# Kernel tuning notes

Hardware: AMD Instinct MI355X
Metric: run time of the kernel (lower is better)

The kernel has to match this reference:

```python
import jax, jax.numpy as jnp
import numpy as np

H = 12      # num_heads
EPS = 1e-5  # LayerNorm eps (torch default)


def _ln(x, g, b):
    m = x.mean(-1, keepdims=True)
    v = x.var(-1, keepdims=True)
    return (x - m) * jax.lax.rsqrt(v + EPS) * g + b


def _rot_half(x):
    x1, x2 = x[..., 0::2], x[..., 1::2]
    return jnp.stack((-x2, x1), axis=-1).reshape(x.shape)


def _rope_tables(n, head_dim):
    # rotary-embedding-torch: RotaryEmbedding(dim=head_dim//2, use_xpos=True),
    # theta=10000, scale_base=512. Only first rot=head_dim//2 dims are rotated.
    rot = head_dim // 2
    inv = 1.0 / (10000.0 ** (jnp.arange(0, rot, 2, dtype=jnp.float32) / rot))
    t = jnp.arange(n, dtype=jnp.float32)
    freqs = jnp.repeat(t[:, None] * inv[None, :], 2, axis=-1)  # (n, rot), interleaved
    base = (jnp.arange(0, rot, 2, dtype=jnp.float32) + 0.4 * rot) / (1.4 * rot)
    power = (t - n // 2) / 512.0
    sc = base[None, :] ** power[:, None]
    sc = jnp.concatenate([sc, sc], axis=-1)  # (n, rot), concatenated (library behavior)
    return jnp.cos(freqs), jnp.sin(freqs), sc


def _attn_path(xn, Wqkv, bqkv, Wproj, bproj, qg, qb, kg, kb, R, rg, rb):
    B, N, D = xn.shape
    d = D // H
    qkv = xn @ Wqkv + bqkv
    q, k, v = jnp.split(qkv, 3, axis=-1)
    hd = lambda t: t.reshape(B, N, H, d).transpose(0, 2, 1, 3)  # (B,H,N,d)
    q, k, v = hd(q), hd(k), hd(v)
    q = _ln(q, qg, qb)  # per-head QK LayerNorm
    k = _ln(k, kg, kb)
    cos, sin, sc = _rope_tables(N, d)
    rot = d // 2

    def rope(t, s):  # rotate only first rot dims
        tl, tr = t[..., :rot], t[..., rot:]
        tl = tl * cos * s + _rot_half(tl) * sin * s
        return jnp.concatenate([tl, tr], axis=-1)

    q = rope(q, sc)
    v = rope(v, 1.0 / sc)  # source applies rope to (q, v), not k

    scores = jnp.einsum('bhid,bhjd->bhij', q, k) / jnp.sqrt(jnp.asarray(d, xn.dtype))
    p = jax.nn.softmax(scores, axis=-1)
    # SDPA(q,k,ones_NN)[...,i,j] == sum_k p[...,i,k] for every j (constant over j).
    # All downstream ops (head-mix einsum, LayerNorm over heads, @ v) therefore
    # reduce exactly to the per-(b,i) computation below, avoiding an N^3 matmul.
    s = p.sum(-1)                              # (B,H,N)
    mix = jnp.einsum('bhi,hg->big', s, R)      # (B,N,H)
    w = _ln(mix, rg, rb)                       # reattn LayerNorm over head axis
    vsum = v.sum(axis=2)                       # (B,H,d); (w @ v) with w const over j
    y = jnp.einsum('big,bgd->bigd', w, vsum).reshape(B, N, D)
    return y @ Wproj + bproj


def _cgmlp(xn, W1, b1, gg, gb, cw, cb, W2, b2):
    h = jax.nn.gelu(xn @ W1 + b1, approximate=False)
    c2 = h.shape[-1] // 2
    xr, xg = h[..., :c2], h[..., c2:]
    xg = _ln(xg, gg, gb).transpose(0, 2, 1)  # (B,C,T)
    K = cw.shape[-1]
    xg = jax.lax.conv_general_dilated(xg, cw, (1,), [((K - 1) // 2, (K - 1) // 2)],
                                      dimension_numbers=('NCH', 'OIH', 'NCH'),
                                      feature_group_count=c2)  # depthwise conv1d
    xg = (xg + cb[None, :, None]).transpose(0, 2, 1)
    return (xr * xg) @ W2 + b2


def reference(x, Wqkv, bqkv, Wproj, bproj, qn_g, qn_b, kn_g, kn_b, reattn_w, rn_g, rn_b,
              ln1_g, ln1_b, ln2_g, ln2_b, ls1, ls2, W1, b1, gn_g, gn_b, conv_w, conv_b,
              W2, b2, Wout, bout):
    # eval mode: dropout / drop_path are identity
    xa = _ln(x, ln1_g, ln1_b)
    attn = sum(_attn_path(xa, Wqkv[p], bqkv[p], Wproj[p], bproj[p], qn_g[p], qn_b[p],
                          kn_g[p], kn_b[p], reattn_w[p], rn_g[p], rn_b[p])
               for p in range(2))
    x_attn = x + ls1 * attn
    xm = _ln(x, ln2_g, ln2_b)
    x_mlp = x + ls2 * _cgmlp(xm, W1, b1, gn_g, gn_b, conv_w, conv_b, W2, b2)
    xf = jnp.concatenate([x_attn, x_mlp], axis=-1)
    return xf @ Wout + bout + x


def setup_inputs():
    B, N, D, P = 4, 1024, 768, 2
    d = D // H
    C = 4 * D
    c2 = C // 2
    K = 21
    ks = iter(jax.random.split(jax.random.key(0), 16))
    nrm = lambda s, sd=0.02: jax.random.normal(next(ks), s, jnp.float32) * sd
    return {
        'x': jax.random.normal(next(ks), (B, N, D), jnp.float32),
        'Wqkv': nrm((P, D, 3 * D)), 'bqkv': jnp.zeros((P, 3 * D)),
        'Wproj': nrm((P, D, D)), 'bproj': jnp.zeros((P, D)),
        'qn_g': jnp.ones((P, d)), 'qn_b': jnp.zeros((P, d)),
        'kn_g': jnp.ones((P, d)), 'kn_b': jnp.zeros((P, d)),
        'reattn_w': jax.random.normal(next(ks), (P, H, H), jnp.float32),
        'rn_g': jnp.ones((P, H)), 'rn_b': jnp.zeros((P, H)),
        'ln1_g': jnp.ones((D,)), 'ln1_b': jnp.zeros((D,)),
        'ln2_g': jnp.ones((D,)), 'ln2_b': jnp.zeros((D,)),
        'ls1': jnp.full((D,), 0.01, jnp.float32), 'ls2': jnp.full((D,), 0.01, jnp.float32),
        'W1': nrm((D, C)), 'b1': jnp.zeros((C,)),
        'gn_g': jnp.ones((c2,)), 'gn_b': jnp.zeros((c2,)),
        'conv_w': nrm((c2, 1, K), 0.1), 'conv_b': jnp.zeros((c2,)),
        'W2': nrm((c2, D)), 'b2': jnp.zeros((D,)),
        'Wout': nrm((2 * D, D)), 'bout': jnp.zeros((D,)),
    }
```

## Files before the change

### kernel.cpp

```cpp
#include <hip/hip_runtime.h>
#include <hip/hip_bf16.h>

typedef short s16x8 __attribute__((ext_vector_type(8)));
typedef float f32x4 __attribute__((ext_vector_type(4)));

#define C2 1536

__device__ __forceinline__ float b2f(ushort u){ return __uint_as_float(((unsigned)u)<<16); }
__device__ __forceinline__ ushort f2b(float f){ unsigned u = __float_as_uint(f); return (ushort)((u + 0x7fffu + ((u>>16)&1u)) >> 16); }

template<int EPI>
__global__ __launch_bounds__(256) void gemm_bf16(
    const ushort* __restrict__ A, const ushort* __restrict__ BT,
    int M, int N, int K,
    const float* __restrict__ bias, const float* __restrict__ scale,
    const float* __restrict__ xres,
    ushort* __restrict__ o16, ushort* __restrict__ o16b, float* __restrict__ o32)
{
    __shared__ ushort Al[2][128*32];
    __shared__ ushort Bl[2][128*32];
    const int t = threadIdx.x;
    const int m0 = blockIdx.y*128, n0 = blockIdx.x*128;
    const int lane = t & 63, wv = t >> 6;
    const int wm = (wv>>1)*64, wn = (wv&1)*64;
    const int r0 = lane & 15, q = lane >> 4;

    const int c0i = t, c1i = t + 256;
    const int lrow0 = ((c0i>>6)<<4) | (c0i&15), lkc0 = ((c0i>>4)&3) << 3;
    const int lrow1 = ((c1i>>6)<<4) | (c1i&15), lkc1 = ((c1i>>4)&3) << 3;
    const ushort* gA0 = A  + (size_t)(m0+lrow0)*K + lkc0;
    const ushort* gB0 = BT + (size_t)(n0+lrow0)*K + lkc0;
    const ushort* gA1 = A  + (size_t)(m0+lrow1)*K + lkc1;
    const ushort* gB1 = BT + (size_t)(n0+lrow1)*K + lkc1;

    f32x4 acc[4][4];
    #pragma unroll
    for (int i=0;i<4;++i)
        #pragma unroll
        for (int j=0;j<4;++j) acc[i][j] = (f32x4){0.f,0.f,0.f,0.f};

    const int nkt = K >> 5;
    uint4 pa0_0, pb0_0, pa1_0, pb1_0;
    uint4 pa0_1, pb0_1, pa1_1, pb1_1;
    pa0_0 = *(const uint4*)gA0;        pb0_0 = *(const uint4*)gB0;
    pa1_0 = *(const uint4*)gA1;        pb1_0 = *(const uint4*)gB1;
    pa0_1 = *(const uint4*)(gA0 + 32); pb0_1 = *(const uint4*)(gB0 + 32);
    pa1_1 = *(const uint4*)(gA1 + 32); pb1_1 = *(const uint4*)(gB1 + 32);
    *(uint4*)&Al[0][c0i*8] = pa0_0;
    *(uint4*)&Bl[0][c0i*8] = pb0_0;
    *(uint4*)&Al[0][c1i*8] = pa1_0;
    *(uint4*)&Bl[0][c1i*8] = pb1_0;

    for (int kt = 0; kt < nkt; kt += 2) {
        __syncthreads();
        {
            s16x8 af[4], bfr[4];
            #pragma unroll
            for (int mt=0; mt<4; ++mt) af[mt]  = *(const s16x8*)&Al[0][(((wm>>4)+mt)*64 + lane)*8];
            #pragma unroll
            for (int nt=0; nt<4; ++nt) bfr[nt] = *(const s16x8*)&Bl[0][(((wn>>4)+nt)*64 + lane)*8];
            *(uint4*)&Al[1][c0i*8] = pa0_1;
            *(uint4*)&Bl[1][c0i*8] = pb0_1;
            *(uint4*)&Al[1][c1i*8] = pa1_1;
            *(uint4*)&Bl[1][c1i*8] = pb1_1;
            if (kt+2 < nkt) {
                pa0_0 = *(const uint4*)(gA0 + (kt+2)*32);
                pb0_0 = *(const uint4*)(gB0 + (kt+2)*32);
                pa1_0 = *(const uint4*)(gA1 + (kt+2)*32);
                pb1_0 = *(const uint4*)(gB1 + (kt+2)*32);
            }
            #pragma unroll
            for (int mt=0; mt<4; ++mt)
                #pragma unroll
                for (int nt=0; nt<4; ++nt)
                    acc[mt][nt] = __builtin_amdgcn_mfma_f32_16x16x32_bf16(af[mt], bfr[nt], acc[mt][nt], 0,0,0);
        }
        __syncthreads();
        {
            s16x8 af[4], bfr[4];
            #pragma unroll
            for (int mt=0; mt<4; ++mt) af[mt]  = *(const s16x8*)&Al[1][(((wm>>4)+mt)*64 + lane)*8];
            #pragma unroll
            for (int nt=0; nt<4; ++nt) bfr[nt] = *(const s16x8*)&Bl[1][(((wn>>4)+nt)*64 + lane)*8];
            if (kt+2 < nkt) {
                *(uint4*)&Al[0][c0i*8] = pa0_0;
                *(uint4*)&Bl[0][c0i*8] = pb0_0;
                *(uint4*)&Al[0][c1i*8] = pa1_0;
                *(uint4*)&Bl[0][c1i*8] = pb1_0;
            }
            if (kt+3 < nkt) {
                pa0_1 = *(const uint4*)(gA0 + (kt+3)*32);
                pb0_1 = *(const uint4*)(gB0 + (kt+3)*32);
                pa1_1 = *(const uint4*)(gA1 + (kt+3)*32);
                pb1_1 = *(const uint4*)(gB1 + (kt+3)*32);
            }
            #pragma unroll
            for (int mt=0; mt<4; ++mt)
                #pragma unroll
                for (int nt=0; nt<4; ++nt)
                    acc[mt][nt] = __builtin_amdgcn_mfma_f32_16x16x32_bf16(af[mt], bfr[nt], acc[mt][nt], 0,0,0);
        }
    }

    #pragma unroll
    for (int mt=0; mt<4; ++mt) {
        #pragma unroll
        for (int nt=0; nt<4; ++nt) {
            int col = n0 + wn + nt*16 + r0;
            #pragma unroll
            for (int r=0; r<4; ++r) {
                int row = m0 + wm + mt*16 + q*4 + r;
                float v = acc[mt][nt][r];
                if (EPI == 0) {
                    o16[(size_t)row*N + col] = f2b(v + bias[col]);
                } else if (EPI == 1) {
                    v += bias[col];
                    float g = 0.5f*v*(1.0f + erff(v*0.70710678118f));
                    if (col < C2) o16 [(size_t)row*C2 + col]        = f2b(g);
                    else          o16b[(size_t)row*C2 + (col - C2)] = f2b(g);
                } else if (EPI == 2) {
                    v += bias[col];
                    o16[(size_t)row*1536 + 768 + col] = f2b(xres[(size_t)row*768 + col] + scale[col]*v);
                } else {
                    o32[(size_t)row*768 + col] = v + bias[col] + xres[(size_t)row*768 + col];
                }
            }
        }
    }
}

__global__ __launch_bounds__(256) void pack_bt(const float* __restrict__ src, ushort* __restrict__ dst,
                                               int K, int ld, int coff)
{
    __shared__ float tl[32*33];
    int kt = blockIdx.x*32, nt = blockIdx.y*32;
    int nl = threadIdx.x & 31, kg = threadIdx.x >> 5;
    #pragma unroll
    for (int kk=0; kk<4; ++kk) {
        int k = kg*4 + kk;
        tl[k*33 + nl] = src[(size_t)(kt + k)*ld + coff + nt + nl];
    }
    __syncthreads();
    int kcol = threadIdx.x & 31, ng = threadIdx.x >> 5;
    #pragma unroll
    for (int nn=0; nn<4; ++nn) {
        int nrow = ng*4 + nn;
        dst[(size_t)(nt + nrow)*K + kt + kcol] = f2b(tl[kcol*33 + nrow]);
    }
}

__global__ __launch_bounds__(256) void pack_bv(const float* __restrict__ bqkv, float* __restrict__ bvp)
{
    int idx = blockIdx.x*256 + threadIdx.x;
    if (idx < 1536) bvp[idx] = bqkv[(idx/768)*2304 + 1536 + (idx%768)];
}

__global__ __launch_bounds__(256) void ln_x_kernel(const float* __restrict__ x,
    const float* __restrict__ g1, const float* __restrict__ b1,
    const float* __restrict__ g2, const float* __restrict__ b2,
    ushort* __restrict__ xa, ushort* __restrict__ xm)
{
    __shared__ float sb[8];
    int row = blockIdx.x; int t = threadIdx.x;
    float v[3]; float s = 0.f, ss = 0.f;
    #pragma unroll
    for (int e=0; e<3; ++e) { v[e] = x[(size_t)row*768 + t + e*256]; s += v[e]; ss += v[e]*v[e]; }
    for (int o=32; o>0; o>>=1){ s += __shfl_down(s,o,64); ss += __shfl_down(ss,o,64); }
    int lane = t&63, w = t>>6;
    if (lane==0){ sb[w]=s; sb[4+w]=ss; }
    __syncthreads();
    s = sb[0]+sb[1]+sb[2]+sb[3]; ss = sb[4]+sb[5]+sb[6]+sb[7];
    float mean = s*(1.f/768.f);
    float var  = ss*(1.f/768.f) - mean*mean;
    float rstd = rsqrtf(var + 1e-5f);
    #pragma unroll
    for (int e=0; e<3; ++e){
        int c = t + e*256;
        float n = (v[e]-mean)*rstd;
        xa[(size_t)row*768 + c] = f2b(n*g1[c] + b1[c]);
        xm[(size_t)row*768 + c] = f2b(n*g2[c] + b2[c]);
    }
}

__global__ __launch_bounds__(256) void prep_kernel(
    float* __restrict__ w1t, float* __restrict__ w2t, float* __restrict__ wvec,
    float* __restrict__ attn_c, float* __restrict__ vsum,
    const float* __restrict__ R, const float* __restrict__ rng,
    const float* __restrict__ rnb, const float* __restrict__ bproj)
{
    int idx = blockIdx.x*256 + threadIdx.x;
    {
        int i = idx >> 6, j = idx & 63;
        float w1, w2;
        if (j < 32) {
            int m = j >> 1;
            float inv = powf(10000.f, -(float)m*(1.f/16.f));
            float fr = (float)i * inv;
            float c = cosf(fr), sn = sinf(fr);
            float power = ((float)i - 512.f) * (1.f/512.f);
            float basev = (2.f*(float)(j & 15) + 12.8f) * (1.f/44.8f);
            float sfac = powf(basev, -power);
            w1 = c * sfac;
            w2 = ((j & 1) ? sn : -sn) * sfac;
        } else { w1 = 1.f; w2 = 0.f; }
        w1t[idx] = w1; w2t[idx] = w2;
    }
    if (blockIdx.x >= 1 && blockIdx.x <= 12) {
        int k = (blockIdx.x-1)*256 + threadIdx.x;
        int o = k % 768;
        attn_c[k] = bproj[o] + bproj[768 + o];
    }
    if (blockIdx.x >= 13 && blockIdx.x <= 36) {
        int k = (blockIdx.x-13)*256 + threadIdx.x;
        vsum[k] = 0.f;
    }
    if (blockIdx.x == 0) {
        __shared__ float mixs[24];
        __shared__ float ws[24];
        int t = threadIdx.x;
        if (t < 24) {
            int p = t / 12, g = t % 12;
            float m = 0.f;
            for (int h=0; h<12; ++h) m += R[p*144 + h*12 + g];
            mixs[t] = m;
        }
        __syncthreads();
        if (t < 2) {
            float mean=0.f, var=0.f;
            for (int g=0; g<12; ++g) mean += mixs[t*12+g];
            mean *= (1.f/12.f);
            for (int g=0; g<12; ++g){ float d = mixs[t*12+g]-mean; var += d*d; }
            var *= (1.f/12.f);
            float rstd = rsqrtf(var + 1e-5f);
            for (int g=0; g<12; ++g)
                ws[t*12+g] = (mixs[t*12+g]-mean)*rstd*rng[t*12+g] + rnb[t*12+g];
        }
        __syncthreads();
        if (t < 24) wvec[t] = ws[t];
    }
}

__global__ __launch_bounds__(256) void rope_reduce(const ushort* __restrict__ V,
    const float* __restrict__ w1t, const float* __restrict__ w2t, float* __restrict__ vsum)
{
    int col = blockIdx.x*256 + threadIdx.x;
    int b = blockIdx.y;
    int i0 = blockIdx.z * 256;
    int j = col & 63;
    float acc = 0.f;
    const ushort* vp = V + (size_t)(b*1024 + i0)*1536;
    #pragma unroll 4
    for (int i=0; i<256; ++i) {
        float v1 = b2f(vp[(size_t)i*1536 + col]);
        float v2 = b2f(vp[(size_t)i*1536 + (col^1)]);
        int ii = i0 + i;
        acc += w1t[ii*64 + j]*v1 + w2t[ii*64 + j]*v2;
    }
    atomicAdd(&vsum[b*1536 + col], acc);
}

__global__ __launch_bounds__(256) void attn_gemm(const float* __restrict__ vsum,
    const float* __restrict__ wvec, const float* __restrict__ Wproj, float* __restrict__ attn_c)
{
    int o  = blockIdx.x*256 + threadIdx.x;
    int c0 = blockIdx.y * 96;
    int b  = blockIdx.z;
    int p  = c0 / 768;
    float acc = 0.f;
    #pragma unroll 4
    for (int cc=0; cc<96; ++cc) {
        int c = c0 + cc;
        int cl = c - p*768;
        float y = wvec[p*12 + (cl>>6)] * vsum[b*1536 + c];
        acc += y * Wproj[(size_t)p*589824 + (size_t)cl*768 + o];
    }
    atomicAdd(&attn_c[b*768 + o], acc);
}

__global__ __launch_bounds__(256) void xf_left(const float* __restrict__ x, const float* __restrict__ ls1,
    const float* __restrict__ attn_c, ushort* __restrict__ xf)
{
    int col = blockIdx.x*256 + threadIdx.x;
    int row = blockIdx.y;
    xf[(size_t)row*1536 + col] = f2b(x[(size_t)row*768 + col] + ls1[col]*attn_c[(row>>10)*768 + col]);
}

__global__ __launch_bounds__(256) void ln_gate(const ushort* __restrict__ xg,
    const float* __restrict__ g, const float* __restrict__ bta, ushort* __restrict__ out)
{
    __shared__ float sb[8];
    int row = blockIdx.x, t = threadIdx.x;
    float v[6]; float s=0.f, ss=0.f;
    #pragma unroll
    for (int e=0;e<6;++e){ v[e] = b2f(xg[(size_t)row*1536 + t + e*256]); s+=v[e]; ss+=v[e]*v[e]; }
    for (int o=32; o>0; o>>=1){ s += __shfl_down(s,o,64); ss += __shfl_down(ss,o,64); }
    int lane = t&63, w = t>>6;
    if (lane==0){ sb[w]=s; sb[4+w]=ss; }
    __syncthreads();
    s = sb[0]+sb[1]+sb[2]+sb[3]; ss = sb[4]+sb[5]+sb[6]+sb[7];
    float mean = s*(1.f/1536.f);
    float var  = ss*(1.f/1536.f) - mean*mean;
    float rstd = rsqrtf(var + 1e-5f);
    #pragma unroll
    for (int e=0;e<6;++e){
        int c = t + e*256;
        out[(size_t)row*1536 + c] = f2b((v[e]-mean)*rstd*g[c] + bta[c]);
    }
}

#define CROWS 128
#define CIN   (CROWS + 20)
#define CSTR  72
__global__ __launch_bounds__(256) void conv_mul(const ushort* __restrict__ xgln,
    const float* __restrict__ cw, const float* __restrict__ cb,
    const ushort* __restrict__ xr, ushort* __restrict__ u)
{
    __shared__ ushort tile[CIN * CSTR];
    const int c0 = blockIdx.x * 64;
    const int i0 = blockIdx.y * CROWS;
    const int b  = blockIdx.z;
    const int t  = threadIdx.x;
    const size_t base = (size_t)b*1024*1536;

    #pragma unroll
    for (int it = 0; it < 5; ++it) {
        int idx = it*256 + t;
        if (idx < CIN*8) {
            int r  = idx >> 3;
            int cq = (idx & 7) * 8;
            int si = i0 + r - 10;
            uint4 val = make_uint4(0u,0u,0u,0u);
            if (si >= 0 && si < 1024)
                val = *(const uint4*)(xgln + base + (size_t)si*1536 + c0 + cq);
            *(uint4*)&tile[r*CSTR + cq] = val;
        }
    }
    __syncthreads();

    const int ch = t & 63;
    const int o0 = (t >> 6) * 32;
    const int c  = c0 + ch;

    float w[21];
    #pragma unroll
    for (int k=0; k<21; ++k) w[k] = cw[c*21 + k];
    const float bias = cb[c];

    float win[21];
    #pragma unroll
    for (int j=0; j<20; ++j) win[j] = b2f(tile[(o0+j)*CSTR + ch]);

    #pragma unroll
    for (int j=0; j<32; ++j) {
        win[(j+20)%21] = b2f(tile[(o0+j+20)*CSTR + ch]);
        float acc = bias;
        #pragma unroll
        for (int k=0; k<21; ++k) acc += win[(j+k)%21] * w[k];
        size_t off = base + (size_t)(i0+o0+j)*1536 + c;
        u[off] = f2b(b2f(xr[off]) * acc);
    }
}

extern "C" void kernel_launch(void* const* d_in, const int* in_sizes, int n_in,
                              void* d_out, int out_size, void* d_ws, size_t ws_size,
                              hipStream_t stream)
{
    const float* x     = (const float*)d_in[0];
    const float* Wqkv  = (const float*)d_in[1];
    const float* bqkv  = (const float*)d_in[2];
    const float* Wproj = (const float*)d_in[3];
    const float* bproj = (const float*)d_in[4];
    const float* Rw    = (const float*)d_in[9];
    const float* rng   = (const float*)d_in[10];
    const float* rnb   = (const float*)d_in[11];
    const float* ln1g  = (const float*)d_in[12];
    const float* ln1b  = (const float*)d_in[13];
    const float* ln2g  = (const float*)d_in[14];
    const float* ln2b  = (const float*)d_in[15];
    const float* ls1   = (const float*)d_in[16];
    const float* ls2   = (const float*)d_in[17];
    const float* W1    = (const float*)d_in[18];
    const float* b1    = (const float*)d_in[19];
    const float* gng   = (const float*)d_in[20];
    const float* gnb   = (const float*)d_in[21];
    const float* cw    = (const float*)d_in[22];
    const float* cb    = (const float*)d_in[23];
    const float* W2    = (const float*)d_in[24];
    const float* b2    = (const float*)d_in[25];
    const float* Wout  = (const float*)d_in[26];
    const float* bout  = (const float*)d_in[27];
    float* out = (float*)d_out;

    char* ws = (char*)d_ws;
    size_t off = 0;
    auto alloc = [&](size_t bytes)->char* {
        char* p = ws + off;
        off += (bytes + 255) & ~(size_t)255;
        return p;
    };
    ushort* WvT   = (ushort*)alloc(1536*768*2);
    ushort* W1T   = (ushort*)alloc(3072*768*2);
    ushort* W2T   = (ushort*)alloc(768*1536*2);
    ushort* WoutT = (ushort*)alloc(768*1536*2);
    float*  bvp   = (float*)alloc(1536*4);
    float*  w1t   = (float*)alloc(65536*4);
    float*  w2t   = (float*)alloc(65536*4);
    float*  wvec  = (float*)alloc(24*4);
    float*  attnc = (float*)alloc(3072*4);
    float*  vsum  = (float*)alloc(6144*4);
    ushort* xa16  = (ushort*)alloc(4096*768*2);
    ushort* xm16  = (ushort*)alloc(4096*768*2);
    ushort* V16   = (ushort*)alloc(4096*1536*2);
    ushort* xg16  = (ushort*)alloc(4096*1536*2);
    ushort* xf16  = (ushort*)alloc(4096*1536*2);
    ushort* xgln  = xa16;
    ushort* xr16  = V16;
    ushort* u16   = xg16;
    (void)ws_size; (void)n_in; (void)in_sizes; (void)out_size;

    for (int p = 0; p < 2; ++p)
        pack_bt<<<dim3(24, 24), 256, 0, stream>>>(Wqkv + (size_t)p*768*2304, WvT + (size_t)p*768*768,
                                                  768, 2304, 1536);
    pack_bt<<<dim3(24, 96), 256, 0, stream>>>(W1,   W1T,   768,  3072, 0);
    pack_bt<<<dim3(48, 24), 256, 0, stream>>>(W2,   W2T,   1536, 768,  0);
    pack_bt<<<dim3(48, 24), 256, 0, stream>>>(Wout, WoutT, 1536, 768,  0);
    pack_bv<<<dim3(6), 256, 0, stream>>>(bqkv, bvp);
    prep_kernel<<<dim3(256), 256, 0, stream>>>(w1t, w2t, wvec, attnc, vsum, Rw, rng, rnb, bproj);

    ln_x_kernel<<<dim3(4096), 256, 0, stream>>>(x, ln1g, ln1b, ln2g, ln2b, xa16, xm16);

    gemm_bf16<0><<<dim3(12, 32), 256, 0, stream>>>(xa16, WvT, 4096, 1536, 768,
                                                   bvp, nullptr, nullptr, V16, nullptr, nullptr);
    rope_reduce<<<dim3(6, 4, 4), 256, 0, stream>>>(V16, w1t, w2t, vsum);
    attn_gemm<<<dim3(3, 16, 4), 256, 0, stream>>>(vsum, wvec, Wproj, attnc);
    xf_left<<<dim3(3, 4096), 256, 0, stream>>>(x, ls1, attnc, xf16);

    gemm_bf16<1><<<dim3(24, 32), 256, 0, stream>>>(xm16, W1T, 4096, 3072, 768,
                                                   b1, nullptr, nullptr, xr16, xg16, nullptr);
    ln_gate<<<dim3(4096), 256, 0, stream>>>(xg16, gng, gnb, xgln);
    conv_mul<<<dim3(24, 8, 4), 256, 0, stream>>>(xgln, cw, cb, xr16, u16);
    gemm_bf16<2><<<dim3(6, 32), 256, 0, stream>>>(u16, W2T, 4096, 768, 1536,
                                                  b2, ls2, x, xf16, nullptr, nullptr);
    gemm_bf16<3><<<dim3(6, 32), 256, 0, stream>>>(xf16, WoutT, 4096, 768, 1536,
                                                  bout, nullptr, x, nullptr, nullptr, out);
}
```

Baseline: 363.6 us.

## Add 256x256 tile GEMM with direct global-to-LDS loads for V and W1 projections

Adds a new 512-thread GEMM kernel that computes 256x256 output tiles with K-step 64, loading A and B straight into 128 KB of dynamic LDS through global_load_lds. It uses XOR-swizzled LDS addressing, a hand-written ping-pong pipeline with explicit waitcnt, barriers and setprio, and 8x4 MFMA accumulators per wave. The V projection and the W1+GELU GEMM switch to it, and the old kernel keeps only the residual epilogues. The aim is more operand reuse per loaded byte and overlap of loads with MFMA work. In exchange the grids get much smaller (96 and 192 blocks on a 256-CU part), so fewer CUs are busy, and register use is high.

After: 367.4 us. No clear change (+1.0%).

```diff
diff --git a/kernel.cpp b/kernel.cpp
--- a/kernel.cpp
+++ b/kernel.cpp
@@ -8,6 +8,155 @@
 
 __device__ __forceinline__ float b2f(ushort u){ return __uint_as_float(((unsigned)u)<<16); }
 __device__ __forceinline__ ushort f2b(float f){ unsigned u = __float_as_uint(f); return (ushort)((u + 0x7fffu + ((u>>16)&1u)) >> 16); }
+
+#define GL16(g, l) __builtin_amdgcn_global_load_lds( \
+    (const __attribute__((address_space(1))) void*)(g), \
+    (__attribute__((address_space(3))) void*)(l), 16, 0, 0)
+
+#define VMW(n) asm volatile("s_waitcnt vmcnt(" #n ")" ::: "memory")
+#define LGW()  asm volatile("s_waitcnt lgkmcnt(0)" ::: "memory")
+#define SB()   __builtin_amdgcn_sched_barrier(0)
+#define BAR()  __builtin_amdgcn_s_barrier()
+#define SP1    __builtin_amdgcn_s_setprio(1)
+#define SP0    __builtin_amdgcn_s_setprio(0)
+#define MF(va, vb, c) __builtin_amdgcn_mfma_f32_16x16x32_bf16(va, vb, c, 0,0,0)
+
+#define RDA(P, mh) { const int ab = (P) + aro + (mh)*4096; \
+    a0=L8(ab+sx0);      a1=L8(ab+sx1); \
+    a2=L8(ab+1024+sx0); a3=L8(ab+1024+sx1); \
+    a4=L8(ab+2048+sx0); a5=L8(ab+2048+sx1); \
+    a6=L8(ab+3072+sx0); a7=L8(ab+3072+sx1); }
+#define RDB0(P, nh) { const int bb = (P) + bro + (nh)*2048; \
+    b00=L8(bb+sx0); b01=L8(bb+sx1); b02=L8(bb+1024+sx0); b03=L8(bb+1024+sx1); }
+#define RDB1(P, nh) { const int bb = (P) + bro + (nh)*2048; \
+    b10=L8(bb+sx0); b11=L8(bb+sx1); b12=L8(bb+1024+sx0); b13=L8(bb+1024+sx1); }
+#define L8(off) (*(const s16x8*)&lds[off])
+#define STG(p0, p1, T, dstb) { \
+    GL16((p0) + (size_t)(T)*64, &lds[(dstb) + ldsw]); \
+    GL16((p1) + (size_t)(T)*64, &lds[(dstb) + 4096 + ldsw]); }
+#define QD(mh, nh, B0,B1,B2,B3) { \
+  acc[(mh)*4+0][(nh)*2+0]=MF(a0,B0,acc[(mh)*4+0][(nh)*2+0]); \
+  acc[(mh)*4+0][(nh)*2+0]=MF(a1,B1,acc[(mh)*4+0][(nh)*2+0]); \
+  acc[(mh)*4+0][(nh)*2+1]=MF(a0,B2,acc[(mh)*4+0][(nh)*2+1]); \
+  acc[(mh)*4+0][(nh)*2+1]=MF(a1,B3,acc[(mh)*4+0][(nh)*2+1]); \
+  acc[(mh)*4+1][(nh)*2+0]=MF(a2,B0,acc[(mh)*4+1][(nh)*2+0]); \
+  acc[(mh)*4+1][(nh)*2+0]=MF(a3,B1,acc[(mh)*4+1][(nh)*2+0]); \
+  acc[(mh)*4+1][(nh)*2+1]=MF(a2,B2,acc[(mh)*4+1][(nh)*2+1]); \
+  acc[(mh)*4+1][(nh)*2+1]=MF(a3,B3,acc[(mh)*4+1][(nh)*2+1]); \
+  acc[(mh)*4+2][(nh)*2+0]=MF(a4,B0,acc[(mh)*4+2][(nh)*2+0]); \
+  acc[(mh)*4+2][(nh)*2+0]=MF(a5,B1,acc[(mh)*4+2][(nh)*2+0]); \
+  acc[(mh)*4+2][(nh)*2+1]=MF(a4,B2,acc[(mh)*4+2][(nh)*2+1]); \
+  acc[(mh)*4+2][(nh)*2+1]=MF(a5,B3,acc[(mh)*4+2][(nh)*2+1]); \
+  acc[(mh)*4+3][(nh)*2+0]=MF(a6,B0,acc[(mh)*4+3][(nh)*2+0]); \
+  acc[(mh)*4+3][(nh)*2+0]=MF(a7,B1,acc[(mh)*4+3][(nh)*2+0]); \
+  acc[(mh)*4+3][(nh)*2+1]=MF(a6,B2,acc[(mh)*4+3][(nh)*2+1]); \
+  acc[(mh)*4+3][(nh)*2+1]=MF(a7,B3,acc[(mh)*4+3][(nh)*2+1]); }
+
+#define EIGHT(t0, t1, DS, VM4) \
+   VMW(4); BAR(); SB(); \
+  RDA(0,0); RDB0(0,0); \
+  STG(pA00,pA01,(t1), 16384); \
+  LGW(); SB(); SP1; QD(0,0,b00,b01,b02,b03); SP0; SB(); BAR(); SB(); \
+   RDB1(0,1); \
+  STG(pA10,pA11,(t1), 24576); \
+  BAR(); SB(); LGW(); SB(); SP1; QD(0,1,b10,b11,b12,b13); SP0; SB(); BAR(); SB(); \
+   RDA(0,1); \
+  if (DS) { STG(pB00,pB01,(t0)+2, 32768); } \
+  BAR(); SB(); LGW(); SB(); SP1; QD(1,0,b00,b01,b02,b03); SP0; SB(); BAR(); SB(); \
+   if (DS) { STG(pB10,pB11,(t0)+2, 40960); } \
+  BAR(); SB(); SP1; QD(1,1,b10,b11,b12,b13); SP0; SB(); BAR(); SB(); \
+   VM4; BAR(); SB(); \
+  RDA(16384,0); RDB0(16384,0); \
+  if (DS) { STG(pA00,pA01,(t0)+2, 0); } \
+  LGW(); SB(); SP1; QD(0,0,b00,b01,b02,b03); SP0; SB(); BAR(); SB(); \
+   RDB1(16384,1); \
+  if (DS) { STG(pA10,pA11,(t0)+2, 8192); } \
+  BAR(); SB(); LGW(); SB(); SP1; QD(0,1,b10,b11,b12,b13); SP0; SB(); BAR(); SB(); \
+   RDA(16384,1); \
+  if (DS) { STG(pB00,pB01,(t1)+2, 49152); } \
+  BAR(); SB(); LGW(); SB(); SP1; QD(1,0,b00,b01,b02,b03); SP0; SB(); BAR(); SB(); \
+   if (DS) { STG(pB10,pB11,(t1)+2, 57344); } \
+  BAR(); SB(); SP1; QD(1,1,b10,b11,b12,b13); SP0; SB(); BAR(); SB();
+
+template<int EPI>
+__global__ __launch_bounds__(512) void gemm256(
+    const ushort* __restrict__ A, const ushort* __restrict__ BT,
+    int M, int N, int K,
+    const float* __restrict__ bias,
+    ushort* __restrict__ o16, ushort* __restrict__ o16b)
+{
+    extern __shared__ ushort lds[];
+    const int t = threadIdx.x;
+    const int lane = t & 63, wv = t >> 6;
+    const int wr = wv >> 2, wc = wv & 3;
+    const int r0 = lane & 15, q = lane >> 4, e7 = lane & 7;
+    const int m0 = blockIdx.y*256, n0 = blockIdx.x*256;
+
+    const int idx = wv*64 + lane;
+    const int lr8 = idx >> 3;
+    const int ksrc = (idx & 7) ^ (lr8 & 7);
+    const ushort* pA00 = A  + (size_t)(m0 +   0 +  0 + lr8)*K + ksrc*8;
+    const ushort* pA01 = A  + (size_t)(m0 +   0 + 64 + lr8)*K + ksrc*8;
+    const ushort* pA10 = A  + (size_t)(m0 + 128 +  0 + lr8)*K + ksrc*8;
+    const ushort* pA11 = A  + (size_t)(m0 + 128 + 64 + lr8)*K + ksrc*8;
+    const ushort* pB00 = BT + (size_t)(n0 +   0 +  0 + lr8)*K + ksrc*8;
+    const ushort* pB01 = BT + (size_t)(n0 +   0 + 64 + lr8)*K + ksrc*8;
+    const ushort* pB10 = BT + (size_t)(n0 + 128 +  0 + lr8)*K + ksrc*8;
+    const ushort* pB11 = BT + (size_t)(n0 + 128 + 64 + lr8)*K + ksrc*8;
+    const int ldsw = wv*512;
+
+    const int aro = (wr*128 + r0)*64;
+    const int bro = 32768 + (wc*64 + r0)*64;
+    const int sx0 = (q ^ e7)*8, sx1 = ((q ^ e7)*8) ^ 32;
+
+    f32x4 acc[8][4];
+    #pragma unroll
+    for (int i=0;i<8;++i)
+        #pragma unroll
+        for (int j=0;j<4;++j) acc[i][j] = (f32x4){0.f,0.f,0.f,0.f};
+    s16x8 a0,a1,a2,a3,a4,a5,a6,a7;
+    s16x8 b00,b01,b02,b03, b10,b11,b12,b13;
+
+    const int nkt = K >> 6;
+    const int niter = nkt >> 1;
+
+    STG(pB00,pB01, 0, 32768);
+    STG(pB10,pB11, 0, 40960);
+    STG(pA00,pA01, 0, 0);
+    STG(pA10,pA11, 0, 8192);
+    STG(pB00,pB01, 1, 49152);
+    STG(pB10,pB11, 1, 57344);
+
+    for (int i = 0; i < niter-1; ++i) {
+        const int t0 = 2*i, t1 = 2*i+1;
+        EIGHT(t0, t1, 1, VMW(4));
+    }
+    {
+        const int t0 = nkt-2, t1 = nkt-1;
+        EIGHT(t0, t1, 0, VMW(0));
+    }
+
+    #pragma unroll
+    for (int gm=0; gm<8; ++gm) {
+        #pragma unroll
+        for (int gn=0; gn<4; ++gn) {
+            int col = n0 + wc*64 + gn*16 + r0;
+            #pragma unroll
+            for (int r=0; r<4; ++r) {
+                int row = m0 + wr*128 + gm*16 + q*4 + r;
+                float v = acc[gm][gn][r];
+                if (EPI == 0) {
+                    o16[(size_t)row*N + col] = f2b(v + bias[col]);
+                } else {
+                    v += bias[col];
+                    float g = 0.5f*v*(1.0f + erff(v*0.70710678118f));
+                    if (col < C2) o16 [(size_t)row*C2 + col]        = f2b(g);
+                    else          o16b[(size_t)row*C2 + (col - C2)] = f2b(g);
+                }
+            }
+        }
+    }
+}
 
 template<int EPI>
 __global__ __launch_bounds__(256) void gemm_bf16(
@@ -15,7 +164,7 @@
     int M, int N, int K,
     const float* __restrict__ bias, const float* __restrict__ scale,
     const float* __restrict__ xres,
-    ushort* __restrict__ o16, ushort* __restrict__ o16b, float* __restrict__ o32)
+    ushort* __restrict__ o16, float* __restrict__ o32)
 {
     __shared__ ushort Al[2][128*32];
     __shared__ ushort Bl[2][128*32];
@@ -111,14 +260,7 @@
             for (int r=0; r<4; ++r) {
                 int row = m0 + wm + mt*16 + q*4 + r;
                 float v = acc[mt][nt][r];
-                if (EPI == 0) {
-                    o16[(size_t)row*N + col] = f2b(v + bias[col]);
-                } else if (EPI == 1) {
-                    v += bias[col];
-                    float g = 0.5f*v*(1.0f + erff(v*0.70710678118f));
-                    if (col < C2) o16 [(size_t)row*C2 + col]        = f2b(g);
-                    else          o16b[(size_t)row*C2 + (col - C2)] = f2b(g);
-                } else if (EPI == 2) {
+                if (EPI == 2) {
                     v += bias[col];
                     o16[(size_t)row*1536 + 768 + col] = f2b(xres[(size_t)row*768 + col] + scale[col]*v);
                 } else {
@@ -418,6 +560,9 @@
     ushort* u16   = xg16;
     (void)ws_size; (void)n_in; (void)in_sizes; (void)out_size;
 
+    (void)hipFuncSetAttribute((const void*)gemm256<0>, hipFuncAttributeMaxDynamicSharedMemorySize, 131072);
+    (void)hipFuncSetAttribute((const void*)gemm256<1>, hipFuncAttributeMaxDynamicSharedMemorySize, 131072);
+
     for (int p = 0; p < 2; ++p)
         pack_bt<<<dim3(24, 24), 256, 0, stream>>>(Wqkv + (size_t)p*768*2304, WvT + (size_t)p*768*768,
                                                   768, 2304, 1536);
@@ -429,18 +574,18 @@
 
     ln_x_kernel<<<dim3(4096), 256, 0, stream>>>(x, ln1g, ln1b, ln2g, ln2b, xa16, xm16);
 
-    gemm_bf16<0><<<dim3(12, 32), 256, 0, stream>>>(xa16, WvT, 4096, 1536, 768,
-                                                   bvp, nullptr, nullptr, V16, nullptr, nullptr);
+    gemm256<0><<<dim3(6, 16), 512, 131072, stream>>>(xa16, WvT, 4096, 1536, 768,
+                                                     bvp, V16, nullptr);
     rope_reduce<<<dim3(6, 4, 4), 256, 0, stream>>>(V16, w1t, w2t, vsum);
     attn_gemm<<<dim3(3, 16, 4), 256, 0, stream>>>(vsum, wvec, Wproj, attnc);
     xf_left<<<dim3(3, 4096), 256, 0, stream>>>(x, ls1, attnc, xf16);
 
-    gemm_bf16<1><<<dim3(24, 32), 256, 0, stream>>>(xm16, W1T, 4096, 3072, 768,
-                                                   b1, nullptr, nullptr, xr16, xg16, nullptr);
+    gemm256<1><<<dim3(12, 16), 512, 131072, stream>>>(xm16, W1T, 4096, 3072, 768,
+                                                      b1, xr16, xg16);
     ln_gate<<<dim3(4096), 256, 0, stream>>>(xg16, gng, gnb, xgln);
     conv_mul<<<dim3(24, 8, 4), 256, 0, stream>>>(xgln, cw, cb, xr16, u16);
     gemm_bf16<2><<<dim3(6, 32), 256, 0, stream>>>(u16, W2T, 4096, 768, 1536,
-                                                  b2, ls2, x, xf16, nullptr, nullptr);
+                                                  b2, ls2, x, xf16, nullptr);
     gemm_bf16<3><<<dim3(6, 32), 256, 0, stream>>>(xf16, WoutT, 4096, 768, 1536,
-                                                  bout, nullptr, x, nullptr, nullptr, out);
-}
+                                                  bout, nullptr, x, nullptr, out);
+}
```
